# Performance work log

Hardware: AMD Instinct MI355X
Metric: run time of the kernel (lower is better)

The kernel has to match this reference:

```python
import jax, jax.numpy as jnp
import numpy as np

B, N_FRAMES, C, S = 4, 32, 256, 16
D = 512            # attn_dim = min(C*S*S, 512)
NHEADS = 8
TOKEN = C * S * S  # 65536
EPS = 1e-5


def _layer_norm_last(x, g, b):
    mu = x.mean(-1, keepdims=True)
    var = x.var(-1, keepdims=True)
    return (x - mu) * jax.lax.rsqrt(var + EPS) * g + b


def _forward(feat, Wp, bp, Wu, bu, Wq, bq, Wk, bk, Wv, bv, Wo, bo, ln1_g, ln1_b,
             Wk1, bk1, Wk2, bk2, Wpc, bpc, gn_g, gn_b, Wf1, bf1, Wf2, bf2,
             dn_g, dn_b, num_frames):
    BN, Cc, H, W = feat.shape
    N = num_frames
    Bb = BN // N
    # 1) flatten frames to tokens and project (B, N, token_dim) -> (B, N, D)
    tokens = feat.reshape(Bb, N, Cc * H * W)
    tp = tokens @ Wp.T + bp
    # contextual grouping with clamped indices: K = v_{n-1}, Q = v_n, V = v_{n+1}
    idx = jnp.arange(N)
    v_prev = tp[:, jnp.maximum(idx - 1, 0)]
    v_next = tp[:, jnp.minimum(idx + 1, N - 1)]
    # 2) MHA with seq_len 1 for Q/K/V (degenerate softmax over a single key)
    dh = D // NHEADS
    q = (tp @ Wq.T + bq).reshape(Bb, N, NHEADS, dh)
    k = (v_prev @ Wk.T + bk).reshape(Bb, N, NHEADS, dh)
    v = (v_next @ Wv.T + bv).reshape(Bb, N, NHEADS, dh)
    scores = jnp.sum(q * k, axis=-1, keepdims=True) / jnp.sqrt(jnp.float32(dh))  # (B,N,h,1)
    wts = jax.nn.softmax(scores, axis=-1)  # identically 1.0 (single key)
    attn = (wts * v).reshape(Bb, N, D) @ Wo.T + bo
    enh = _layer_norm_last(attn + tp, ln1_g, ln1_b)
    # 3) unproject back to feature maps
    feat_attn = (enh @ Wu.T + bu).reshape(BN, Cc, H, W)
    # 4) DynamicConv: per-sample depthwise 3x3 kernels conditioned on GAP
    gap = feat_attn.mean((2, 3))                       # (BN, C)
    hid = jax.nn.relu(gap @ Wk1.T + bk1)
    kern = (hid @ Wk2.T + bk2).reshape(BN, Cc, 3, 3)   # per-sample, per-channel kernels
    xp = jnp.pad(feat_attn, ((0, 0), (0, 0), (1, 1), (1, 1)))
    out = jnp.zeros_like(feat_attn)
    for di in range(3):  # fixed 3x3 kernel taps
        for dj in range(3):
            out = out + kern[:, :, di, dj][:, :, None, None] * xp[:, :, di:di + H, dj:dj + W]
    # 1x1 proj conv
    out = jnp.einsum('nchw,dc->ndhw', out, Wpc) + bpc[:, None, None]
    # GroupNorm(min(32,C))
    G = min(32, Cc)
    og = out.reshape(BN, G, -1)
    mu = og.mean(-1, keepdims=True)
    var = og.var(-1, keepdims=True)
    out = ((og - mu) * jax.lax.rsqrt(var + EPS)).reshape(BN, Cc, H, W)
    feat_dc = out * gn_g[:, None, None] + gn_b[:, None, None]
    # 5) dc_fc (1x1 conv -> relu -> 1x1 conv) + residual, then LayerNorm([C,S,S])
    y = jax.nn.relu(jnp.einsum('nchw,dc->ndhw', feat_dc, Wf1) + bf1[:, None, None])
    y = jnp.einsum('nchw,dc->ndhw', y, Wf2) + bf2[:, None, None]
    z = y + feat_attn
    zf = z.reshape(BN, -1)
    mu = zf.mean(-1, keepdims=True)
    var = zf.var(-1, keepdims=True)
    zn = ((zf - mu) * jax.lax.rsqrt(var + EPS)).reshape(BN, Cc, H, W)
    return zn * dn_g + dn_b


def setup_inputs() -> dict:
    key = jax.random.key(0)
    ks = jax.random.split(key, 16)
    sc = 0.02
    inp = {
        'feat': jax.random.normal(ks[0], (B * N_FRAMES, C, S, S), jnp.float32),
        'Wp': jax.random.normal(ks[1], (D, TOKEN), jnp.float32) * sc,
        'bp': jnp.zeros((D,), jnp.float32),
        'Wu': jax.random.normal(ks[2], (TOKEN, D), jnp.float32) * sc,
        'bu': jnp.zeros((TOKEN,), jnp.float32),
        'Wq': jax.random.normal(ks[3], (D, D), jnp.float32) * sc,
        'bq': jnp.zeros((D,), jnp.float32),
        'Wk': jax.random.normal(ks[4], (D, D), jnp.float32) * sc,
        'bk': jnp.zeros((D,), jnp.float32),
        'Wv': jax.random.normal(ks[5], (D, D), jnp.float32) * sc,
        'bv': jnp.zeros((D,), jnp.float32),
        'Wo': jax.random.normal(ks[6], (D, D), jnp.float32) * sc,
        'bo': jnp.zeros((D,), jnp.float32),
        'ln1_g': jnp.ones((D,), jnp.float32),
        'ln1_b': jnp.zeros((D,), jnp.float32),
        'Wk1': jax.random.normal(ks[7], (C, C), jnp.float32) * sc,
        'bk1': jnp.zeros((C,), jnp.float32),
        'Wk2': jax.random.normal(ks[8], (C * 9, C), jnp.float32) * sc,
        'bk2': jnp.zeros((C * 9,), jnp.float32),
        'Wpc': jax.random.normal(ks[9], (C, C), jnp.float32) * sc,
        'bpc': jnp.zeros((C,), jnp.float32),
        'gn_g': jnp.ones((C,), jnp.float32),
        'gn_b': jnp.zeros((C,), jnp.float32),
        'Wf1': jax.random.normal(ks[10], (C, C), jnp.float32) * sc,
        'bf1': jnp.zeros((C,), jnp.float32),
        'Wf2': jax.random.normal(ks[11], (C, C), jnp.float32) * sc,
        'bf2': jnp.zeros((C,), jnp.float32),
        'dn_g': jnp.ones((C, S, S), jnp.float32),
        'dn_b': jnp.zeros((C, S, S), jnp.float32),
        'num_frames': N_FRAMES,
    }
    return inp


def reference(feat, Wp, bp, Wu, bu, Wq, bq, Wk, bk, Wv, bv, Wo, bo, ln1_g, ln1_b,
              Wk1, bk1, Wk2, bk2, Wpc, bpc, gn_g, gn_b, Wf1, bf1, Wf2, bf2,
              dn_g, dn_b, num_frames):
    return _forward(feat, Wp, bp, Wu, bu, Wq, bq, Wk, bk, Wv, bv, Wo, bo,
                    ln1_g, ln1_b, Wk1, bk1, Wk2, bk2, Wpc, bpc, gn_g, gn_b,
                    Wf1, bf1, Wf2, bf2, dn_g, dn_b, num_frames)
```

## Files before the change

### kernel.cpp

```cpp
#include <hip/hip_runtime.h>


typedef unsigned short u16;
typedef unsigned int u32;
typedef __attribute__((ext_vector_type(8))) short short8;
typedef __attribute__((ext_vector_type(4))) float floatx4;

__device__ __forceinline__ float b2f(u16 h){ return __uint_as_float(((u32)h)<<16); }
__device__ __forceinline__ u16 f2b(float f){
  u32 u = __float_as_uint(f);
  u = (u + 0x7FFFu + ((u>>16)&1u)) >> 16;
  return (u16)u;
}
__device__ __forceinline__ u32 cvtpk(float lo, float hi){
  u32 r;
  asm("v_cvt_pk_bf16_f32 %0, %1, %2" : "=v"(r) : "v"(lo), "v"(hi));
  return r;
}
__device__ __forceinline__ float blo(u32 w){ return __uint_as_float(w<<16); }
__device__ __forceinline__ float bhi(u32 w){ return __uint_as_float(w & 0xFFFF0000u); }
__device__ __forceinline__ bool probe_f32(const u32* p){ return p[0]==0x3F800000u; }

__device__ __forceinline__ float wred(float v){
  #pragma unroll
  for (int o=32;o>0;o>>=1) v += __shfl_down(v, o, 64);
  return v;
}

__device__ __forceinline__ float dot8(uint4 u, const float* t){
  return t[0]*blo(u.x)+t[1]*bhi(u.x)+t[2]*blo(u.y)+t[3]*bhi(u.y)
       + t[4]*blo(u.z)+t[5]*bhi(u.z)+t[6]*blo(u.w)+t[7]*bhi(u.w);
}

__device__ __forceinline__ void bar_lgkm(){
  asm volatile("s_waitcnt lgkmcnt(0)" ::: "memory");
  __builtin_amdgcn_sched_barrier(0);
  __builtin_amdgcn_s_barrier();
  asm volatile("" ::: "memory");
}

struct SrcTab { const void* p[22]; };

__global__ __launch_bounds__(256) void cvt_k(SrcTab st, const u32* probe, u16* dst){
  constexpr int ns[22]   = {262144,262144,65536,589824,65536,65536,65536,65536,65536,
                            65536,512,512,512,512,512,256,2304,256,256,256,256,256};
  constexpr int offs[22] = {0,262144,524288,589824,1179648,1245184,1310720,1376256,1441792,
                            1507328,1572864,1573376,1573888,1574400,1574912,1575424,1575680,
                            1577984,1578240,1578496,1578752,1579008};
  int t = blockIdx.y;
  int e = (blockIdx.x*256 + threadIdx.x)*4;
  if (e >= ns[t]) return;
  u16* d = dst + offs[t] + e;
  if (probe_f32(probe)){
    float4 v = *(const float4*)((const float*)st.p[t] + e);
    d[0]=f2b(v.x); d[1]=f2b(v.y); d[2]=f2b(v.z); d[3]=f2b(v.w);
  } else {
    *(uint2*)d = *(const uint2*)((const u16*)st.p[t] + e);
  }
}

template<int MODE>
__global__ __launch_bounds__(256) void gemm_k(
    const void* __restrict__ Ap, int lda,
    const void* __restrict__ Bp, int ldb,
    void* __restrict__ Cp, int N, int Ktot, int kchunk,
    const u16* __restrict__ bias,
    const float* __restrict__ gnst,
    const u16* __restrict__ gng, const u16* __restrict__ gnb,
    const u16* __restrict__ fres,
    const u32* __restrict__ probe, int araw, int braw)
{
  __shared__ __align__(16) u16 As0[64*72];
  __shared__ __align__(16) u16 Bs0[64*72];
  __shared__ __align__(16) u16 As1[64*72];
  __shared__ __align__(16) u16 Bs1[64*72];

  const bool pf32 = probe_f32(probe);
  const bool a32 = araw && pf32, b32 = braw && pf32;

  const int tid = threadIdx.x;
  const int lane = tid & 63, wv = tid >> 6;
  const int mw = wv >> 1, nw = wv & 1;
  const int m0 = blockIdx.x * 64, n0 = blockIdx.y * 64;
  int k0 = 0, kend = Ktot;
  if (MODE == 0) { k0 = blockIdx.z * kchunk; kend = k0 + kchunk; }

  floatx4 zf = {0.f,0.f,0.f,0.f};
  floatx4 acc[2][2];
  acc[0][0]=zf; acc[0][1]=zf; acc[1][0]=zf; acc[1][1]=zf;

  const int ml = lane & 15, q = lane >> 4;
  const int ar0 = (mw*32 + ml)*72 + q*8;
  const int ar1 = ar0 + 16*72;
  const int br0 = (nw*32 + ml)*72 + q*8;
  const int br1 = br0 + 16*72;

  const int row0 = tid >> 3, colc = tid & 7;

  auto ld_tiles = [&](uint4 (&pa)[2][2], uint4 (&pb)[2][2], int kk){
    #pragma unroll
    for (int i=0;i<2;i++){
      int row = row0 + i*32;
      if (a32){
        const float* s = (const float*)Ap + (size_t)(m0+row)*lda + kk + colc*8;
        pa[i][0] = ((const uint4*)s)[0];
        pa[i][1] = ((const uint4*)s)[1];
      } else {
        const u16* s = (const u16*)Ap + (size_t)(m0+row)*lda + kk + colc*8;
        pa[i][0] = *(const uint4*)s;
      }
      if (b32){
        const float* s = (const float*)Bp + (size_t)(n0+row)*ldb + kk + colc*8;
        pb[i][0] = ((const uint4*)s)[0];
        pb[i][1] = ((const uint4*)s)[1];
      } else {
        const u16* s = (const u16*)Bp + (size_t)(n0+row)*ldb + kk + colc*8;
        pb[i][0] = *(const uint4*)s;
      }
    }
  };

  auto stage = [&](uint4 (&pa)[2][2], uint4 (&pb)[2][2], int kk, u16* As, u16* Bs){
    #pragma unroll
    for (int i=0;i<2;i++){
      int row = row0 + i*32;
      u16* adst = &As[row*72 + colc*8];
      if (MODE == 3){
        uint4 u = pa[i][0];
        int nsamp = (m0+row) >> 8;
        int cbase = kk + colc*8;
        int g = cbase >> 3;
        float mu = gnst[(nsamp*32+g)*2], rs = gnst[(nsamp*32+g)*2+1];
        float f[8] = {blo(u.x),bhi(u.x),blo(u.y),bhi(u.y),blo(u.z),bhi(u.z),blo(u.w),bhi(u.w)};
        float fn[8];
        #pragma unroll
        for (int j=0;j<8;j++){
          int c = cbase + j;
          fn[j] = (f[j]-mu)*rs*b2f(gng[c]) + b2f(gnb[c]);
        }
        uint4 t4;
        t4.x = cvtpk(fn[0],fn[1]); t4.y = cvtpk(fn[2],fn[3]);
        t4.z = cvtpk(fn[4],fn[5]); t4.w = cvtpk(fn[6],fn[7]);
        *(uint4*)adst = t4;
      } else if (a32){
        uint4 v0 = pa[i][0], v1 = pa[i][1];
        uint4 t4;
        t4.x = cvtpk(__uint_as_float(v0.x), __uint_as_float(v0.y));
        t4.y = cvtpk(__uint_as_float(v0.z), __uint_as_float(v0.w));
        t4.z = cvtpk(__uint_as_float(v1.x), __uint_as_float(v1.y));
        t4.w = cvtpk(__uint_as_float(v1.z), __uint_as_float(v1.w));
        *(uint4*)adst = t4;
      } else {
        *(uint4*)adst = pa[i][0];
      }
      u16* bdst = &Bs[row*72 + colc*8];
      if (b32){
        uint4 v0 = pb[i][0], v1 = pb[i][1];
        uint4 t4;
        t4.x = cvtpk(__uint_as_float(v0.x), __uint_as_float(v0.y));
        t4.y = cvtpk(__uint_as_float(v0.z), __uint_as_float(v0.w));
        t4.z = cvtpk(__uint_as_float(v1.x), __uint_as_float(v1.y));
        t4.w = cvtpk(__uint_as_float(v1.z), __uint_as_float(v1.w));
        *(uint4*)bdst = t4;
      } else {
        *(uint4*)bdst = pb[i][0];
      }
    }
  };

  auto mfma_step = [&](const u16* As, const u16* Bs){
    #pragma unroll
    for (int ks2=0; ks2<2; ks2++){
      int ko = ks2*32;
      short8 a0 = *(const short8*)&As[ar0 + ko];
      short8 a1 = *(const short8*)&As[ar1 + ko];
      short8 b0 = *(const short8*)&Bs[br0 + ko];
      short8 b1 = *(const short8*)&Bs[br1 + ko];
      acc[0][0] = __builtin_amdgcn_mfma_f32_16x16x32_bf16(a0, b0, acc[0][0], 0,0,0);
      acc[0][1] = __builtin_amdgcn_mfma_f32_16x16x32_bf16(a0, b1, acc[0][1], 0,0,0);
      acc[1][0] = __builtin_amdgcn_mfma_f32_16x16x32_bf16(a1, b0, acc[1][0], 0,0,0);
      acc[1][1] = __builtin_amdgcn_mfma_f32_16x16x32_bf16(a1, b1, acc[1][1], 0,0,0);
    }
  };

  uint4 pa0[2][2], pb0[2][2], pa1[2][2], pb1[2][2];
  ld_tiles(pa0, pb0, k0);
  ld_tiles(pa1, pb1, k0 + 64);
  for (int kk = k0; kk < kend; kk += 128){
    stage(pa0, pb0, kk, As0, Bs0);
    if (kk + 128 < kend) ld_tiles(pa0, pb0, kk + 128);
    bar_lgkm();
    mfma_step(As0, Bs0);
    stage(pa1, pb1, kk + 64, As1, Bs1);
    if (kk + 192 < kend) ld_tiles(pa1, pb1, kk + 192);
    bar_lgkm();
    mfma_step(As1, Bs1);
  }

  const int colg = lane & 15, quad = lane >> 4;
  #pragma unroll
  for (int mi=0;mi<2;mi++){
    #pragma unroll
    for (int ni=0;ni<2;ni++){
      #pragma unroll
      for (int r=0;r<4;r++){
        int m = m0 + mw*32 + mi*16 + quad*4 + r;
        int n = n0 + nw*32 + ni*16 + colg;
        float v = acc[mi][ni][r];
        if (MODE==0){
          atomicAdd(&((float*)Cp)[(size_t)m*N + n], v);
        } else if (MODE==1){
          ((u16*)Cp)[(size_t)m*N + n] = f2b(v + b2f(bias[n]));
        } else if (MODE==3){
          ((u16*)Cp)[(size_t)m*N + n] = f2b(fmaxf(v + b2f(bias[n]), 0.f));
        } else if (MODE==4){
          int nsp = m >> 8, s = m & 255;
          ((u16*)Cp)[(size_t)m*N + n] =
              f2b(v + b2f(bias[n]) + b2f(fres[(size_t)nsp*65536 + (size_t)n*256 + s]));
        }
      }
    }
  }
}

__global__ __launch_bounds__(512) void attn_ln_k(
    const float* __restrict__ tp, const u16* __restrict__ Wv, const u16* __restrict__ bv,
    const u16* __restrict__ Wo, const u16* __restrict__ bo, const u16* __restrict__ bp,
    const u16* __restrict__ g, const u16* __restrict__ bln, u16* __restrict__ enh)
{
  __shared__ float tpr[512], tpn[512], vv[512], red[16];
  int r = blockIdx.x; int n = r & 31; int rn = (n==31) ? r : r+1;
  int t = threadIdx.x;
  float bpv = b2f(bp[t]);
  tpr[t] = tp[(size_t)r*512 + t] + bpv;
  tpn[t] = tp[(size_t)rn*512 + t] + bpv;
  __syncthreads();
  {
    const uint4* w4 = (const uint4*)(Wv + (size_t)t*512);
    float acc = b2f(bv[t]);
    #pragma unroll 8
    for (int i=0;i<64;i++) acc += dot8(w4[i], &tpn[i*8]);
    vv[t] = acc;
  }
  __syncthreads();
  float x;
  {
    const uint4* w4 = (const uint4*)(Wo + (size_t)t*512);
    float acc = b2f(bo[t]);
    #pragma unroll 8
    for (int i=0;i<64;i++) acc += dot8(w4[i], &vv[i*8]);
    x = acc + tpr[t];
  }
  float s1 = wred(x), s2 = wred(x*x);
  int lane = t & 63, wid = t >> 6;
  if (lane==0){ red[wid] = s1; red[8+wid] = s2; }
  __syncthreads();
  if (t==0){
    float a=0.f, b=0.f;
    #pragma unroll
    for (int i=0;i<8;i++){ a += red[i]; b += red[8+i]; }
    float mu = a/512.f; float var = b/512.f - mu*mu;
    red[0]=mu; red[1]=rsqrtf(var+1e-5f);
  }
  __syncthreads();
  float mu = red[0], rs = red[1];
  enh[(size_t)r*512 + t] = f2b((x-mu)*rs*b2f(g[t]) + b2f(bln[t]));
}

__global__ __launch_bounds__(256) void gap_k(const u16* __restrict__ fa, float* __restrict__ gapb){
  int wid = threadIdx.x>>6, lane = threadIdx.x&63;
  int pair = blockIdx.x*4 + wid;
  const uint2* p = (const uint2*)(fa + (size_t)pair*256);
  uint2 v = p[lane];
  float s = wred(blo(v.x)+bhi(v.x)+blo(v.y)+bhi(v.y));
  if (lane==0) gapb[pair] = s * (1.0f/256.0f);
}

__global__ __launch_bounds__(256) void hidkern_k(
    const float* __restrict__ gapb, const u16* __restrict__ Wk1, const u16* __restrict__ bk1,
    const u16* __restrict__ Wk2, const u16* __restrict__ bk2, float* __restrict__ kernb)
{
  __shared__ float gl[256], hl[256];
  int nn = blockIdx.x, t = threadIdx.x;
  gl[t] = gapb[(size_t)nn*256 + t];
  __syncthreads();
  {
    const uint4* w4 = (const uint4*)(Wk1 + (size_t)t*256);
    float acc = b2f(bk1[t]);
    #pragma unroll 8
    for (int i=0;i<32;i++) acc += dot8(w4[i], &gl[i*8]);
    hl[t] = fmaxf(acc, 0.f);
  }
  __syncthreads();
  for (int qq=0; qq<9; qq++){
    int e = t*9 + qq;
    const uint4* w4 = (const uint4*)(Wk2 + (size_t)e*256);
    float acc = b2f(bk2[e]);
    #pragma unroll 8
    for (int i=0;i<32;i++) acc += dot8(w4[i], &hl[i*8]);
    kernb[(size_t)nn*2304 + e] = acc;
  }
}

__global__ __launch_bounds__(256) void conv_k(
    const u16* __restrict__ fa, const float* __restrict__ kernb, u16* __restrict__ dwb)
{
  int b = blockIdx.x; int h = b & 15; int nn = b >> 4; int c = threadIdx.x;
  float kv[9];
  #pragma unroll
  for (int qq=0; qq<9; qq++) kv[qq] = kernb[(size_t)nn*2304 + c*9 + qq];
  float rowv[3][18];
  #pragma unroll
  for (int di=0; di<3; di++){
    int hh = h + di - 1;
    if (hh >= 0 && hh < 16){
      const u16* rp = fa + (size_t)nn*65536 + (size_t)c*256 + hh*16;
      rowv[di][0] = 0.f; rowv[di][17] = 0.f;
      #pragma unroll
      for (int w=0; w<16; w++) rowv[di][w+1] = b2f(rp[w]);
    } else {
      #pragma unroll
      for (int x=0; x<18; x++) rowv[di][x] = 0.f;
    }
  }
  #pragma unroll
  for (int w=0; w<16; w++){
    float o = 0.f;
    #pragma unroll
    for (int di=0; di<3; di++)
      o += kv[di*3]*rowv[di][w] + kv[di*3+1]*rowv[di][w+1] + kv[di*3+2]*rowv[di][w+2];
    dwb[((size_t)nn*256 + h*16 + w)*256 + c] = f2b(o);
  }
}

__global__ __launch_bounds__(256) void gnstats_k(const u16* __restrict__ out2, float* __restrict__ gnst){
  int wid = threadIdx.x>>6, lane = threadIdx.x&63;
  int grp = blockIdx.x*4 + wid; int nn = grp >> 5; int gg = grp & 31;
  const u16* base = out2 + (size_t)nn*65536 + gg*8;
  float s=0.f, ss=0.f;
  #pragma unroll 4
  for (int i=0;i<32;i++){
    int f = i*64 + lane; int sidx = f >> 3; int j = f & 7;
    float v = b2f(base[(size_t)sidx*256 + j]);
    s += v; ss += v*v;
  }
  s = wred(s); ss = wred(ss);
  if (lane==0){
    float mu = s/2048.f; float var = ss/2048.f - mu*mu;
    gnst[grp*2] = mu; gnst[grp*2+1] = rsqrtf(var + 1e-5f);
  }
}

__global__ __launch_bounds__(256) void lnstats_k(const u16* __restrict__ z, float* __restrict__ lnst){
  __shared__ float red[8];
  int nn = blockIdx.x, t = threadIdx.x;
  const uint4* p = (const uint4*)(z + (size_t)nn*65536);
  float s=0.f, ss=0.f;
  for (int i=0;i<32;i++){
    uint4 v = p[(size_t)i*256 + t];
    float f0=blo(v.x),f1=bhi(v.x),f2=blo(v.y),f3=bhi(v.y);
    float f4=blo(v.z),f5=bhi(v.z),f6=blo(v.w),f7=bhi(v.w);
    s  += (f0+f1)+(f2+f3)+(f4+f5)+(f6+f7);
    ss += (f0*f0+f1*f1)+(f2*f2+f3*f3)+(f4*f4+f5*f5)+(f6*f6+f7*f7);
  }
  s = wred(s); ss = wred(ss);
  int lane = t&63, wid = t>>6;
  if (lane==0){ red[wid]=s; red[4+wid]=ss; }
  __syncthreads();
  if (t==0){
    float a=red[0]+red[1]+red[2]+red[3];
    float b=red[4]+red[5]+red[6]+red[7];
    float mu = a/65536.f; float var = b/65536.f - mu*mu;
    lnst[nn*2] = mu; lnst[nn*2+1] = rsqrtf(var + 1e-5f);
  }
}

__global__ __launch_bounds__(256) void final_k(
    const u16* __restrict__ z, const float* __restrict__ lnst,
    const u16* __restrict__ dng, const u16* __restrict__ dnb,
    void* __restrict__ outp, const u32* __restrict__ probe)
{
  __shared__ float zt[32*257];
  const bool pf32 = probe_f32(probe);
  int b = blockIdx.x; int nn = b >> 3; int s0 = (b & 7)*32;
  int t = threadIdx.x;
  {
    int srow = t >> 3; int c0 = (t & 7)*32;
    const uint4* p = (const uint4*)(z + (size_t)nn*65536 + (size_t)(s0+srow)*256 + c0);
    float* dst = &zt[srow*257 + c0];
    #pragma unroll
    for (int i=0;i<4;i++){
      uint4 v = p[i];
      dst[i*8+0]=blo(v.x); dst[i*8+1]=bhi(v.x); dst[i*8+2]=blo(v.y); dst[i*8+3]=bhi(v.y);
      dst[i*8+4]=blo(v.z); dst[i*8+5]=bhi(v.z); dst[i*8+6]=blo(v.w); dst[i*8+7]=bhi(v.w);
    }
  }
  __syncthreads();
  float mu = lnst[nn*2], rs = lnst[nn*2+1];
  int sl = t & 31, cq = t >> 5;
  for (int i=0;i<32;i++){
    int c = i*8 + cq;
    float v = (zt[sl*257 + c] - mu) * rs;
    int gidx = c*256 + s0 + sl;
    float res = v*b2f(dng[gidx]) + b2f(dnb[gidx]);
    size_t oi = (size_t)nn*65536 + gidx;
    if (pf32) ((float*)outp)[oi] = res;
    else      ((u16*)outp)[oi]   = f2b(res);
  }
}

extern "C" void kernel_launch(void* const* d_in, const int* in_sizes, int n_in,
                              void* d_out, int out_size, void* d_ws, size_t ws_size,
                              hipStream_t stream) {
  (void)in_sizes; (void)n_in; (void)out_size; (void)ws_size;
  const u32* probe = (const u32*)d_in[21];

  char* w = (char*)d_ws;
  u16* cvt = (u16*)w;
  u16 *cWv  = cvt+0,       *cWo  = cvt+262144, *cWk1 = cvt+524288, *cWk2 = cvt+589824;
  u16 *cWpc = cvt+1179648, *cWf1 = cvt+1245184,*cWf2 = cvt+1310720;
  u16 *cdng = cvt+1376256, *cdnb = cvt+1441792,*cbu  = cvt+1507328;
  u16 *cbp  = cvt+1572864, *cbv  = cvt+1573376,*cbo  = cvt+1573888;
  u16 *cln1g= cvt+1574400, *cln1b= cvt+1574912,*cbk1 = cvt+1575424,*cbk2 = cvt+1575680;
  u16 *cbpc = cvt+1577984, *cgng = cvt+1578240,*cgnb = cvt+1578496;
  u16 *cbf1 = cvt+1578752, *cbf2 = cvt+1579008;

  float* tp_raw = (float*)(w + 4194304);
  u16*   enh    = (u16*)  (w + 4456448);
  float* gapb   = (float*)(w + 4587520);
  float* kernb  = (float*)(w + 4718592);
  float* gnst   = (float*)(w + 5898240);
  float* lnst   = (float*)(w + 5931008);
  u16*   fa     = (u16*)  (w + 8388608);
  u16*   out2   = (u16*)  (w + 25165824);
  u16*   z      = out2;
  u16*   dwb    = (u16*)d_out;
  u16*   y1     = dwb;

  SrcTab st;
  st.p[0]=d_in[9];  st.p[1]=d_in[11]; st.p[2]=d_in[15]; st.p[3]=d_in[17];
  st.p[4]=d_in[19]; st.p[5]=d_in[23]; st.p[6]=d_in[25]; st.p[7]=d_in[27];
  st.p[8]=d_in[28]; st.p[9]=d_in[4];  st.p[10]=d_in[2]; st.p[11]=d_in[10];
  st.p[12]=d_in[12];st.p[13]=d_in[13];st.p[14]=d_in[14];st.p[15]=d_in[16];
  st.p[16]=d_in[18];st.p[17]=d_in[20];st.p[18]=d_in[21];st.p[19]=d_in[22];
  st.p[20]=d_in[24];st.p[21]=d_in[26];

  cvt_k<<<dim3(576,22), 256, 0, stream>>>(st, probe, cvt);
  hipMemsetAsync(tp_raw, 0, 128*512*4, stream);
  gemm_k<0><<<dim3(2,8,128), 256, 0, stream>>>(d_in[0], 65536, d_in[1], 65536, tp_raw,
      512, 65536, 512, nullptr, nullptr, nullptr, nullptr, nullptr, probe, 1, 1);
  attn_ln_k<<<128, 512, 0, stream>>>(tp_raw, cWv, cbv, cWo, cbo, cbp, cln1g, cln1b, enh);
  gemm_k<1><<<dim3(2,1024,1), 256, 0, stream>>>(enh, 512, d_in[3], 512, fa,
      65536, 512, 0, cbu, nullptr, nullptr, nullptr, nullptr, probe, 0, 1);
  gap_k<<<8192, 256, 0, stream>>>(fa, gapb);
  hidkern_k<<<128, 256, 0, stream>>>(gapb, cWk1, cbk1, cWk2, cbk2, kernb);
  conv_k<<<2048, 256, 0, stream>>>(fa, kernb, dwb);
  gemm_k<1><<<dim3(512,4,1), 256, 0, stream>>>(dwb, 256, cWpc, 256, out2,
      256, 256, 0, cbpc, nullptr, nullptr, nullptr, nullptr, probe, 0, 0);
  gnstats_k<<<1024, 256, 0, stream>>>(out2, gnst);
  gemm_k<3><<<dim3(512,4,1), 256, 0, stream>>>(out2, 256, cWf1, 256, y1,
      256, 256, 0, cbf1, gnst, cgng, cgnb, nullptr, probe, 0, 0);
  gemm_k<4><<<dim3(512,4,1), 256, 0, stream>>>(y1, 256, cWf2, 256, z,
      256, 256, 0, cbf2, nullptr, nullptr, nullptr, fa, probe, 0, 0);
  lnstats_k<<<128, 256, 0, stream>>>(z, lnst);
  final_k<<<1024, 256, 0, stream>>>(z, lnst, cdng, cdnb, d_out, probe);
}
```

Baseline: 630.7 us.

## Use direct global-to-LDS loads for split-K token projection GEMM

Adds a dedicated split-K kernel for the large 128x512x65536 projection GEMM. It loads raw fp32 (or bf16) tiles straight into XOR-swizzled LDS with global_load_lds, converts to bf16 at fragment read time, and uses larger K chunks so fewer blocks issue atomics. The generic GEMM drops to a single LDS buffer with extra barriers, which halves its shared memory and may raise occupancy. The cost is extra synchronisation in the generic GEMM and fp32 data taking twice the LDS bandwidth.

```diff
diff --git a/kernel.cpp b/kernel.cpp
--- a/kernel.cpp
+++ b/kernel.cpp
@@ -21,6 +21,12 @@
 __device__ __forceinline__ float bhi(u32 w){ return __uint_as_float(w & 0xFFFF0000u); }
 __device__ __forceinline__ bool probe_f32(const u32* p){ return p[0]==0x3F800000u; }
 
+__device__ __forceinline__ void gload_lds16(const void* g, void* l){
+  __builtin_amdgcn_global_load_lds(
+      (const __attribute__((address_space(1))) unsigned int*)g,
+      (__attribute__((address_space(3))) unsigned int*)l, 16, 0, 0);
+}
+
 __device__ __forceinline__ float wred(float v){
   #pragma unroll
   for (int o=32;o>0;o>>=1) v += __shfl_down(v, o, 64);
@@ -35,6 +41,11 @@
 __device__ __forceinline__ void bar_lgkm(){
   asm volatile("s_waitcnt lgkmcnt(0)" ::: "memory");
   __builtin_amdgcn_sched_barrier(0);
+  __builtin_amdgcn_s_barrier();
+  asm volatile("" ::: "memory");
+}
+__device__ __forceinline__ void bar(){
+  asm volatile("" ::: "memory");
   __builtin_amdgcn_s_barrier();
   asm volatile("" ::: "memory");
 }
@@ -59,6 +70,137 @@
   }
 }
 
+__global__ __launch_bounds__(256) void gemm32_k(
+    const void* __restrict__ Ap, int lda,
+    const void* __restrict__ Bp, int ldb,
+    float* __restrict__ Cp, int N, int kchunk,
+    const u32* __restrict__ probe)
+{
+  __shared__ __align__(16) char As0[8192];
+  __shared__ __align__(16) char Bs0[8192];
+  __shared__ __align__(16) char As1[8192];
+  __shared__ __align__(16) char Bs1[8192];
+
+  const bool pf32 = probe_f32(probe);
+  const int tid = threadIdx.x;
+  const int lane = tid & 63, wv = tid >> 6;
+  const int mw = wv >> 1, nw = wv & 1;
+  const int m0 = blockIdx.x * 64, n0 = blockIdx.y * 64;
+  const int k0 = blockIdx.z * kchunk, kend = k0 + kchunk;
+
+  floatx4 zf = {0.f,0.f,0.f,0.f};
+  floatx4 acc[2][2];
+  acc[0][0]=zf; acc[0][1]=zf; acc[1][0]=zf; acc[1][1]=zf;
+
+  const int ml = lane & 15, q = lane >> 4;
+
+  auto stage32 = [&](char* As, char* Bs, int kk){
+    #pragma unroll
+    for (int i=0;i<2;i++){
+      int g = wv*2 + i;
+      int ci = g*64 + lane;
+      int row = ci >> 3, slot = ci & 7;
+      int c = slot ^ (row & 7);
+      gload_lds16((const float*)Ap + (size_t)(m0+row)*lda + kk + c*4, As + g*1024);
+      gload_lds16((const float*)Bp + (size_t)(n0+row)*ldb + kk + c*4, Bs + g*1024);
+    }
+  };
+  auto compute32 = [&](const char* As, const char* Bs){
+    short8 af[2], bf2[2];
+    #pragma unroll
+    for (int i=0;i<2;i++){
+      int arow = mw*32 + ml + i*16;
+      int r7 = arow & 7;
+      uint4 u0 = *(const uint4*)(As + arow*128 + ((q*2)   ^ r7)*16);
+      uint4 u1 = *(const uint4*)(As + arow*128 + ((q*2+1) ^ r7)*16);
+      uint4 t;
+      t.x = cvtpk(__uint_as_float(u0.x), __uint_as_float(u0.y));
+      t.y = cvtpk(__uint_as_float(u0.z), __uint_as_float(u0.w));
+      t.z = cvtpk(__uint_as_float(u1.x), __uint_as_float(u1.y));
+      t.w = cvtpk(__uint_as_float(u1.z), __uint_as_float(u1.w));
+      union { uint4 u; short8 s; } ca; ca.u = t; af[i] = ca.s;
+      int brow = nw*32 + ml + i*16;
+      int s7 = brow & 7;
+      uint4 v0 = *(const uint4*)(Bs + brow*128 + ((q*2)   ^ s7)*16);
+      uint4 v1 = *(const uint4*)(Bs + brow*128 + ((q*2+1) ^ s7)*16);
+      uint4 w4;
+      w4.x = cvtpk(__uint_as_float(v0.x), __uint_as_float(v0.y));
+      w4.y = cvtpk(__uint_as_float(v0.z), __uint_as_float(v0.w));
+      w4.z = cvtpk(__uint_as_float(v1.x), __uint_as_float(v1.y));
+      w4.w = cvtpk(__uint_as_float(v1.z), __uint_as_float(v1.w));
+      union { uint4 u; short8 s; } cb; cb.u = w4; bf2[i] = cb.s;
+    }
+    acc[0][0] = __builtin_amdgcn_mfma_f32_16x16x32_bf16(af[0], bf2[0], acc[0][0], 0,0,0);
+    acc[0][1] = __builtin_amdgcn_mfma_f32_16x16x32_bf16(af[0], bf2[1], acc[0][1], 0,0,0);
+    acc[1][0] = __builtin_amdgcn_mfma_f32_16x16x32_bf16(af[1], bf2[0], acc[1][0], 0,0,0);
+    acc[1][1] = __builtin_amdgcn_mfma_f32_16x16x32_bf16(af[1], bf2[1], acc[1][1], 0,0,0);
+  };
+
+  auto stage16 = [&](char* As, char* Bs, int kk){
+    int ci = wv*64 + lane;
+    int row = ci >> 2, slot = ci & 3;
+    int c = slot ^ ((row>>1) & 3);
+    gload_lds16((const u16*)Ap + (size_t)(m0+row)*lda + kk + c*8, As + wv*1024);
+    gload_lds16((const u16*)Bp + (size_t)(n0+row)*ldb + kk + c*8, Bs + wv*1024);
+  };
+  auto compute16 = [&](const char* As, const char* Bs){
+    short8 af[2], bf2[2];
+    #pragma unroll
+    for (int i=0;i<2;i++){
+      int arow = mw*32 + ml + i*16;
+      int sa = q ^ ((arow>>1) & 3);
+      union { uint4 u; short8 s; } ca; ca.u = *(const uint4*)(As + arow*64 + sa*16);
+      af[i] = ca.s;
+      int brow = nw*32 + ml + i*16;
+      int sb = q ^ ((brow>>1) & 3);
+      union { uint4 u; short8 s; } cb; cb.u = *(const uint4*)(Bs + brow*64 + sb*16);
+      bf2[i] = cb.s;
+    }
+    acc[0][0] = __builtin_amdgcn_mfma_f32_16x16x32_bf16(af[0], bf2[0], acc[0][0], 0,0,0);
+    acc[0][1] = __builtin_amdgcn_mfma_f32_16x16x32_bf16(af[0], bf2[1], acc[0][1], 0,0,0);
+    acc[1][0] = __builtin_amdgcn_mfma_f32_16x16x32_bf16(af[1], bf2[0], acc[1][0], 0,0,0);
+    acc[1][1] = __builtin_amdgcn_mfma_f32_16x16x32_bf16(af[1], bf2[1], acc[1][1], 0,0,0);
+  };
+
+  if (pf32){
+    stage32(As0, Bs0, k0);
+    __syncthreads();
+    for (int kk = k0; kk < kend; kk += 64){
+      stage32(As1, Bs1, kk + 32);
+      compute32(As0, Bs0);
+      __syncthreads();
+      if (kk + 64 < kend) stage32(As0, Bs0, kk + 64);
+      compute32(As1, Bs1);
+      __syncthreads();
+    }
+  } else {
+    stage16(As0, Bs0, k0);
+    __syncthreads();
+    for (int kk = k0; kk < kend; kk += 64){
+      stage16(As1, Bs1, kk + 32);
+      compute16(As0, Bs0);
+      __syncthreads();
+      if (kk + 64 < kend) stage16(As0, Bs0, kk + 64);
+      compute16(As1, Bs1);
+      __syncthreads();
+    }
+  }
+
+  const int colg = lane & 15, quad = lane >> 4;
+  #pragma unroll
+  for (int mi=0;mi<2;mi++){
+    #pragma unroll
+    for (int ni=0;ni<2;ni++){
+      #pragma unroll
+      for (int r=0;r<4;r++){
+        int m = m0 + mw*32 + mi*16 + quad*4 + r;
+        int n = n0 + nw*32 + ni*16 + colg;
+        atomicAdd(&Cp[(size_t)m*N + n], acc[mi][ni][r]);
+      }
+    }
+  }
+}
+
 template<int MODE>
 __global__ __launch_bounds__(256) void gemm_k(
     const void* __restrict__ Ap, int lda,
@@ -70,10 +212,8 @@
     const u16* __restrict__ fres,
     const u32* __restrict__ probe, int araw, int braw)
 {
-  __shared__ __align__(16) u16 As0[64*72];
-  __shared__ __align__(16) u16 Bs0[64*72];
-  __shared__ __align__(16) u16 As1[64*72];
-  __shared__ __align__(16) u16 Bs1[64*72];
+  __shared__ __align__(16) u16 As[64*72];
+  __shared__ __align__(16) u16 Bs[64*72];
 
   const bool pf32 = probe_f32(probe);
   const bool a32 = araw && pf32, b32 = braw && pf32;
@@ -83,7 +223,7 @@
   const int mw = wv >> 1, nw = wv & 1;
   const int m0 = blockIdx.x * 64, n0 = blockIdx.y * 64;
   int k0 = 0, kend = Ktot;
-  if (MODE == 0) { k0 = blockIdx.z * kchunk; kend = k0 + kchunk; }
+  (void)kchunk;
 
   floatx4 zf = {0.f,0.f,0.f,0.f};
   floatx4 acc[2][2];
@@ -120,7 +260,7 @@
     }
   };
 
-  auto stage = [&](uint4 (&pa)[2][2], uint4 (&pb)[2][2], int kk, u16* As, u16* Bs){
+  auto stage = [&](uint4 (&pa)[2][2], uint4 (&pb)[2][2], int kk){
     #pragma unroll
     for (int i=0;i<2;i++){
       int row = row0 + i*32;
@@ -168,7 +308,7 @@
     }
   };
 
-  auto mfma_step = [&](const u16* As, const u16* Bs){
+  auto mfma_step = [&](){
     #pragma unroll
     for (int ks2=0; ks2<2; ks2++){
       int ko = ks2*32;
@@ -185,16 +325,17 @@
 
   uint4 pa0[2][2], pb0[2][2], pa1[2][2], pb1[2][2];
   ld_tiles(pa0, pb0, k0);
-  ld_tiles(pa1, pb1, k0 + 64);
   for (int kk = k0; kk < kend; kk += 128){
-    stage(pa0, pb0, kk, As0, Bs0);
+    bar();
+    ld_tiles(pa1, pb1, kk + 64);
+    stage(pa0, pb0, kk);
+    bar_lgkm();
+    mfma_step();
+    bar();
     if (kk + 128 < kend) ld_tiles(pa0, pb0, kk + 128);
+    stage(pa1, pb1, kk + 64);
     bar_lgkm();
-    mfma_step(As0, Bs0);
-    stage(pa1, pb1, kk + 64, As1, Bs1);
-    if (kk + 192 < kend) ld_tiles(pa1, pb1, kk + 192);
-    bar_lgkm();
-    mfma_step(As1, Bs1);
+    mfma_step();
   }
 
   const int colg = lane & 15, quad = lane >> 4;
@@ -207,9 +348,7 @@
         int m = m0 + mw*32 + mi*16 + quad*4 + r;
         int n = n0 + nw*32 + ni*16 + colg;
         float v = acc[mi][ni][r];
-        if (MODE==0){
-          atomicAdd(&((float*)Cp)[(size_t)m*N + n], v);
-        } else if (MODE==1){
+        if (MODE==1){
           ((u16*)Cp)[(size_t)m*N + n] = f2b(v + b2f(bias[n]));
         } else if (MODE==3){
           ((u16*)Cp)[(size_t)m*N + n] = f2b(fmaxf(v + b2f(bias[n]), 0.f));
@@ -447,8 +586,8 @@
 
   cvt_k<<<dim3(576,22), 256, 0, stream>>>(st, probe, cvt);
   hipMemsetAsync(tp_raw, 0, 128*512*4, stream);
-  gemm_k<0><<<dim3(2,8,128), 256, 0, stream>>>(d_in[0], 65536, d_in[1], 65536, tp_raw,
-      512, 65536, 512, nullptr, nullptr, nullptr, nullptr, nullptr, probe, 1, 1);
+  gemm32_k<<<dim3(2,8,64), 256, 0, stream>>>(d_in[0], 65536, d_in[1], 65536, tp_raw,
+      512, 1024, probe);
   attn_ln_k<<<128, 512, 0, stream>>>(tp_raw, cWv, cbv, cWo, cbo, cbp, cln1g, cln1b, enh);
   gemm_k<1><<<dim3(2,1024,1), 256, 0, stream>>>(enh, 512, d_in[3], 512, fa,
       65536, 512, 0, cbu, nullptr, nullptr, nullptr, nullptr, probe, 0, 1);
```

New measurement: 615.7 us. 1.02x faster.
